# Kernel optimization log

Hardware: AMD Instinct MI355X
Metric: run time of the kernel (lower is better)

The kernel has to match this reference:

```python
import jax, jax.numpy as jnp
import numpy as np

B, T, D, E, K = 4, 1024, 512, 10, 2
H = 4 * D          # expert hidden
CITY, CE = 8, 32   # num cities, city embedding dim
LIN = D + CE + D // 4 + D // 4 + D // 8 + D // 8  # 928 router input dim


def setup_inputs() -> dict:
    key = jax.random.key(0)
    ks = jax.random.split(key, 16)
    s = 0.02  # init scale for weights
    return {
        "x": jax.random.normal(ks[0], (B, T, D), jnp.float32),
        "delta_t": jax.random.normal(ks[1], (B, T, D // 4), jnp.float32),
        "delta_dis": jax.random.normal(ks[2], (B, T, D // 4), jnp.float32),
        "delta_rg": jax.random.normal(ks[3], (B, T, D // 8), jnp.float32),
        "delta_entropy": jax.random.normal(ks[4], (B, T, D // 8), jnp.float32),
        "city_emb": jax.random.normal(ks[5], (CITY, CE), jnp.float32),
        "Wg": jax.random.normal(ks[6], (E, LIN), jnp.float32) * s,
        "bg": jnp.zeros((E,), jnp.float32),
        "Wn": jax.random.normal(ks[7], (E, LIN), jnp.float32) * s,
        "bn": jnp.zeros((E,), jnp.float32),
        "W1": jax.random.normal(ks[8], (E, D, H), jnp.float32) * s,
        "b1": jnp.zeros((E, H), jnp.float32),
        "W2": jax.random.normal(ks[9], (E, H, D), jnp.float32) * s,
        "b2": jnp.zeros((E, D), jnp.float32),
        "noise": jax.random.normal(ks[10], (B, T, E), jnp.float32),
        "city": jax.random.randint(ks[11], (B,), 0, CITY),
    }


def reference(x, delta_t, delta_dis, delta_rg, delta_entropy, city_emb,
              Wg, bg, Wn, bn, W1, b1, W2, b2, noise, city):
    # ---- router: concat features -> noisy top-k gating ----
    ce = city_emb[city]                                   # (B, CE)
    ce = jnp.broadcast_to(ce[:, None, :], (x.shape[0], x.shape[1], ce.shape[-1]))
    h = jnp.concatenate([x, ce, delta_t, delta_dis, delta_rg, delta_entropy], axis=-1)  # (B,T,LIN)
    logits = jnp.einsum('btl,el->bte', h, Wg) + bg        # clean gate logits
    gate1 = jax.nn.softmax(logits, axis=-1)               # dense gate (returned for aux loss)
    noise_logits = jnp.einsum('btl,el->bte', h, Wn) + bn
    noisy = logits + noise * jax.nn.softplus(noise_logits)
    _, idx = jax.lax.top_k(noisy, K)                      # (B,T,K)
    sel = jax.nn.one_hot(idx, E, dtype=noisy.dtype).sum(-2) > 0  # (B,T,E) bool
    gating = jax.nn.softmax(jnp.where(sel, noisy, -jnp.inf), axis=-1)  # zeros off top-k

    # ---- experts: dense compute, combine weighted by sparse gate ----
    flat_x = x.reshape(-1, D)                             # (N, D)
    flat_g = gating.reshape(-1, E)                        # (N, E), zero for non-selected
    hid = jax.nn.gelu(jnp.einsum('nd,edh->neh', flat_x, W1) + b1, approximate=False)
    y = jnp.einsum('neh,ehd->ned', hid, W2) + b2          # (N, E, D)
    out = jnp.einsum('ne,ned->nd', flat_g, y).reshape(x.shape)
    return out, gate1
```

## Files before the change

### kernel.cpp

```cpp
#include <hip/hip_runtime.h>
#include <hip/hip_bf16.h>

#define B_      4
#define T_      1024
#define NTOK    4096
#define D_      512
#define E_      10
#define H_      2048
#define LIN_    928
#define TOPK    2
#define BM      128
#define ROWS_CAP 9472
#define TILES_CAP 74

typedef __bf16 bf16x8 __attribute__((ext_vector_type(8)));
typedef float  f32x4  __attribute__((ext_vector_type(4)));
typedef unsigned short ushort8 __attribute__((ext_vector_type(8)));

#define OFF_W1T   0ull
#define SZ_W1T    (10ull*2048*512*2)
#define OFF_W2T   (OFF_W1T + SZ_W1T)
#define SZ_W2T    SZ_W1T
#define OFF_XG    (OFF_W2T + SZ_W2T)
#define SZ_XG     ((size_t)ROWS_CAP*512*2)
#define OFF_HID   (OFF_XG + SZ_XG)
#define SZ_HID    ((size_t)ROWS_CAP*2048*2)
#define OFF_Y     OFF_W1T
#define OFF_TOKE  (OFF_HID + SZ_HID)
#define OFF_TOKG  (OFF_TOKE + 32768)
#define OFF_TROWS (OFF_TOKG + 32768)
#define OFF_RANK  (OFF_TROWS + 32768)
#define OFF_CNT   (OFF_RANK + 32768)

static __device__ __forceinline__ unsigned short f2b(float f) {
  unsigned int u = __float_as_uint(f);
  unsigned int r = (u + 0x7fffu + ((u >> 16) & 1u)) >> 16;
  return (unsigned short)r;
}

static __device__ __forceinline__ float b2f(unsigned short u) {
  return __uint_as_float(((unsigned int)u) << 16);
}

static __device__ __forceinline__ void gld16(const void* g, void* l) {
  __builtin_amdgcn_global_load_lds(
      (const __attribute__((address_space(1))) unsigned int*)g,
      (__attribute__((address_space(3))) unsigned int*)l, 16, 0, 0);
}

struct WconvLds { float t[64][65]; };

static __device__ __forceinline__ void wconv_body(
    const float* __restrict__ src, unsigned short* __restrict__ dst,
    int R, int C, int e, int bx, int by, int tid, WconvLds* W) {
  int c0 = bx << 6, r0 = by << 6;
  int rr = tid >> 4, cc = (tid & 15) << 2;
  const float* s = src + ((size_t)e * R + r0 + rr) * C + c0 + cc;
#pragma unroll
  for (int p = 0; p < 4; p++) {
    float4 v = *(const float4*)(s + (size_t)p * 16 * C);
    W->t[rr + p * 16][cc + 0] = v.x; W->t[rr + p * 16][cc + 1] = v.y;
    W->t[rr + p * 16][cc + 2] = v.z; W->t[rr + p * 16][cc + 3] = v.w;
  }
  __syncthreads();
  int rb = (tid & 7) * 8;
#pragma unroll
  for (int pass = 0; pass < 2; pass++) {
    int wc2 = pass * 32 + (tid >> 3);
    ushort8 o;
#pragma unroll
    for (int i = 0; i < 8; i++) o[i] = f2b(W->t[rb + i][wc2]);
    *(ushort8*)&dst[((size_t)e * C + c0 + wc2) * R + r0 + rb] = o;
  }
}

__global__ __launch_bounds__(256) void prep_k(
    const float* __restrict__ x, const float* __restrict__ dt,
    const float* __restrict__ dd, const float* __restrict__ dr,
    const float* __restrict__ de, const float* __restrict__ cemb,
    const int* __restrict__ city,
    const float* __restrict__ Wg, const float* __restrict__ Wn,
    const float* __restrict__ bg, const float* __restrict__ bn,
    const float* __restrict__ noise,
    const float* __restrict__ W1, const float* __restrict__ W2,
    unsigned short* __restrict__ w1T, unsigned short* __restrict__ w2T,
    float* __restrict__ gate1, int* __restrict__ tok_e,
    float* __restrict__ tok_g, int* __restrict__ ranks,
    int* __restrict__ counts) {
  __shared__ WconvLds W;
  __shared__ int lcnt[E_], lbase[E_];
  int bx = blockIdx.x;
  int tid = threadIdx.x;
  if (bx >= 256) {
    int idx = bx - 256;
    if (idx < 2560) wconv_body(W1, w1T, 512, 2048, idx / 256, idx & 31, (idx >> 5) & 7, tid, &W);
    else { idx -= 2560; wconv_body(W2, w2T, 2048, 512, idx / 256, idx & 7, (idx >> 3) & 31, tid, &W); }
    return;
  }
  if (tid < E_) lcnt[tid] = 0;
  __syncthreads();
  int lane = tid & 63;
  int gw = bx * 4 + (tid >> 6);
  int n0 = gw * 4;
  int cb = city[n0 >> 10];

  float acc[4][20];
#pragma unroll
  for (int j = 0; j < 4; j++)
#pragma unroll
    for (int o = 0; o < 20; o++) acc[j][o] = 0.f;

  {
    float hce = (lane < 32) ? cemb[cb * 32 + lane] : 0.f;
    int c = 512 + (lane & 31);
#pragma unroll
    for (int o = 0; o < 10; o++) {
      float wg = Wg[o * LIN_ + c];
      float wn = Wn[o * LIN_ + c];
#pragma unroll
      for (int j = 0; j < 4; j++) {
        acc[j][o]      = fmaf(hce, wg, acc[j][o]);
        acc[j][10 + o] = fmaf(hce, wn, acc[j][10 + o]);
      }
    }
  }
#pragma unroll
  for (int s = 0; s < 5; s++) {
    const float* hp; int Wd, cofs;
    if      (s == 0) { hp = x;  Wd = 512; cofs = 0;   }
    else if (s == 1) { hp = dt; Wd = 128; cofs = 544; }
    else if (s == 2) { hp = dd; Wd = 128; cofs = 672; }
    else if (s == 3) { hp = dr; Wd = 64;  cofs = 800; }
    else             { hp = de; Wd = 64;  cofs = 864; }
    for (int base = 0; base < Wd; base += 64) {
      int c = cofs + base + lane;
      float wv[20];
#pragma unroll
      for (int o = 0; o < 10; o++) {
        wv[o]      = Wg[o * LIN_ + c];
        wv[10 + o] = Wn[o * LIN_ + c];
      }
      float hv[4];
#pragma unroll
      for (int j = 0; j < 4; j++) hv[j] = hp[(size_t)(n0 + j) * Wd + base + lane];
#pragma unroll
      for (int j = 0; j < 4; j++)
#pragma unroll
        for (int o = 0; o < 20; o++) acc[j][o] = fmaf(hv[j], wv[o], acc[j][o]);
    }
  }
#pragma unroll
  for (int off = 1; off < 64; off <<= 1) {
#pragma unroll
    for (int j = 0; j < 4; j++)
#pragma unroll
      for (int o = 0; o < 20; o++) acc[j][o] += __shfl_xor(acc[j][o], off);
  }
  float sv[20];
#pragma unroll
  for (int o = 0; o < 20; o++) {
    float v = acc[0][o];
    v = (lane == 1) ? acc[1][o] : v;
    v = (lane == 2) ? acc[2][o] : v;
    v = (lane == 3) ? acc[3][o] : v;
    sv[o] = v;
  }
  int n = n0 + lane;
  int i0 = 0, i1 = 0, rr0 = 0, rr1 = 0;
  float gg0 = 0.f, gg1 = 0.f, gate[E_];
#pragma unroll
  for (int o = 0; o < E_; o++) gate[o] = 0.f;
  if (lane < 4) {
    float logits[E_], noisy[E_];
    float mx = -3.4e38f;
#pragma unroll
    for (int o = 0; o < E_; o++) { logits[o] = sv[o] + bg[o]; mx = fmaxf(mx, logits[o]); }
    float ssum = 0.f;
#pragma unroll
    for (int o = 0; o < E_; o++) { gate[o] = expf(logits[o] - mx); ssum += gate[o]; }
    float inv = 1.f / ssum;
#pragma unroll
    for (int o = 0; o < E_; o++) gate[o] *= inv;
#pragma unroll
    for (int o = 0; o < E_; o++) {
      float tt = sv[10 + o] + bn[o];
      float sp = (tt > 20.f) ? tt : log1pf(expf(tt));
      noisy[o] = logits[o] + noise[(size_t)n * E_ + o] * sp;
    }
    float v0 = noisy[0];
#pragma unroll
    for (int o = 1; o < E_; o++) if (noisy[o] > v0) { v0 = noisy[o]; i0 = o; }
    float v1 = -3.4e38f; i1 = -1;
#pragma unroll
    for (int o = 0; o < E_; o++) if (o != i0 && noisy[o] > v1) { v1 = noisy[o]; i1 = o; }
    float ee = expf(v1 - v0);
    gg0 = 1.f / (1.f + ee); gg1 = ee * gg0;
    rr0 = atomicAdd(&lcnt[i0], 1);
    rr1 = atomicAdd(&lcnt[i1], 1);
  }
  __syncthreads();
  if (tid < E_) lbase[tid] = atomicAdd(&counts[tid], lcnt[tid]);
  __syncthreads();
  if (lane < 4) {
    tok_e[2 * n] = i0;  tok_e[2 * n + 1] = i1;
    tok_g[2 * n] = gg0; tok_g[2 * n + 1] = gg1;
    ranks[2 * n]     = lbase[i0] + rr0;
    ranks[2 * n + 1] = lbase[i1] + rr1;
#pragma unroll
    for (int o = 0; o < E_; o++) gate1[(size_t)n * E_ + o] = gate[o];
  }
}

__global__ __launch_bounds__(256) void scatgath_k(
    const float* __restrict__ x, const int* __restrict__ tok_e,
    const int* __restrict__ ranks, const int* __restrict__ counts,
    int* __restrict__ token_rows, unsigned short* __restrict__ xg) {
  int n = blockIdx.x * 4 + (threadIdx.x >> 6);
  int lane = threadIdx.x & 63;
  int e0 = tok_e[2 * n], e1 = tok_e[2 * n + 1];
  int off0 = 0, off1 = 0, off = 0;
#pragma unroll
  for (int k = 0; k < E_; k++) {
    if (k == e0) off0 = off;
    if (k == e1) off1 = off;
    off += ((counts[k] + BM - 1) / BM) * BM;
  }
  int p0 = off0 + ranks[2 * n];
  int p1 = off1 + ranks[2 * n + 1];
  if (lane == 0) { token_rows[2 * n] = p0; token_rows[2 * n + 1] = p1; }
  float4 a = *(const float4*)&x[(size_t)n * D_ + lane * 8];
  float4 b = *(const float4*)&x[(size_t)n * D_ + lane * 8 + 4];
  ushort8 o;
  o[0] = f2b(a.x); o[1] = f2b(a.y); o[2] = f2b(a.z); o[3] = f2b(a.w);
  o[4] = f2b(b.x); o[5] = f2b(b.y); o[6] = f2b(b.z); o[7] = f2b(b.w);
  *(ushort8*)&xg[(size_t)p0 * D_ + lane * 8] = o;
  *(ushort8*)&xg[(size_t)p1 * D_ + lane * 8] = o;
}

template<int KD, int ND, int GX, int MODE>
__global__ __launch_bounds__(256) void gemm_k(
    const unsigned short* __restrict__ A, const unsigned short* __restrict__ BT,
    const float* __restrict__ bias, unsigned short* __restrict__ outb,
    const int* __restrict__ counts) {
  constexpr int BMT = 128, BNT = 128;
  constexpr int NT = KD / 32;
  constexpr int BUFSZ = (BMT + BNT) * 32;
  int nwg = GX * TILES_CAP;
  int fid = blockIdx.y * GX + blockIdx.x;
  int w = (fid & 7) * (nwg >> 3) + (fid >> 3);
  int bxs = w % GX, bys = w / GX;
  int e = -1, row0 = 0;
  {
    int off = 0, tt = 0;
#pragma unroll
    for (int k = 0; k < E_; k++) {
      int nt = (counts[k] + BM - 1) / BM;
      if (bys >= tt && bys < tt + nt) { e = k; row0 = off + (bys - tt) * BM; }
      tt += nt; off += nt * BM;
    }
  }
  if (e < 0) return;
  int n0 = bxs * BNT;
  int tid = threadIdx.x;
  int lane = tid & 63, wid = tid >> 6;
  int wr = wid >> 1, wc = wid & 1;
  __shared__ __align__(16) unsigned short LDS[3][BUFSZ];
  f32x4 acc[4][4] = {};
  const unsigned short* Ab = A + (size_t)row0 * KD;
  const unsigned short* Bb = BT + ((size_t)e * ND + n0) * KD;
  int lrow = lane >> 2, lcol = (lane & 3) * 8;
  int r = lane & 15, g8 = (lane >> 4) * 8;
  const unsigned short* gp[4];
  int loff[4];
#pragma unroll
  for (int i = 0; i < 4; i++) {
    int rowb = (wid + 4 * i) * 16;
    gp[i] = (rowb < BMT) ? Ab + (size_t)(rowb + lrow) * KD + lcol
                         : Bb + (size_t)(rowb - BMT + lrow) * KD + lcol;
    loff[i] = rowb * 32;
  }
  auto stage = [&](int buf) {
    unsigned short* lb = &LDS[0][0] + buf * BUFSZ;
#pragma unroll
    for (int i = 0; i < 4; i++) { gld16(gp[i], lb + loff[i]); gp[i] += 32; }
  };
  stage(0); stage(1);
  int cur = 0, nb = 2;
  for (int t = 0; t < NT; ++t) {
    if (t + 2 < NT) {
      stage(nb);
      asm volatile("s_waitcnt vmcnt(8)" ::: "memory");
    } else if (t + 2 == NT) {
      asm volatile("s_waitcnt vmcnt(4)" ::: "memory");
    } else {
      asm volatile("s_waitcnt vmcnt(0)" ::: "memory");
    }
    asm volatile("s_barrier" ::: "memory");
    const unsigned short* cb2 = &LDS[0][0] + cur * BUFSZ;
    bf16x8 av[4], bv[4];
#pragma unroll
    for (int mi = 0; mi < 4; mi++)
      av[mi] = *(const bf16x8*)&cb2[(wr * 64 + mi * 16 + r) * 32 + g8];
#pragma unroll
    for (int ni = 0; ni < 4; ni++)
      bv[ni] = *(const bf16x8*)&cb2[(BMT + wc * 64 + ni * 16 + r) * 32 + g8];
#pragma unroll
    for (int mi = 0; mi < 4; mi++)
#pragma unroll
      for (int ni = 0; ni < 4; ni++)
        acc[mi][ni] = __builtin_amdgcn_mfma_f32_16x16x32_bf16(av[mi], bv[ni], acc[mi][ni], 0, 0, 0);
    asm volatile("s_barrier" ::: "memory");
    cur = (cur == 2) ? 0 : cur + 1;
    nb = (nb == 2) ? 0 : nb + 1;
  }
  int rq = (lane >> 4) * 4;
#pragma unroll
  for (int mi = 0; mi < 4; mi++) {
#pragma unroll
    for (int ni = 0; ni < 4; ni++) {
      int col = n0 + wc * 64 + ni * 16 + r;
      float bz = (MODE == 0) ? bias[e * ND + col] : 0.f;
#pragma unroll
      for (int q = 0; q < 4; q++) {
        int row = row0 + wr * 64 + mi * 16 + rq + q;
        float v = acc[mi][ni][q];
        if constexpr (MODE == 0) {
          v += bz;
          v = 0.5f * v * (1.f + erff(v * 0.70710678118654752440f));
        }
        outb[(size_t)row * ND + col] = f2b(v);
      }
    }
  }
}

__global__ void combine_k(const unsigned short* __restrict__ y, const float* __restrict__ b2,
                          const int* __restrict__ token_rows, const int* __restrict__ tok_e,
                          const float* __restrict__ tok_g, float* __restrict__ out) {
  int gid = blockIdx.x * 256 + threadIdx.x;
  int n = gid >> 6;
  int c = (gid & 63) << 3;
  int r0 = token_rows[2 * n], r1 = token_rows[2 * n + 1];
  int e0 = tok_e[2 * n], e1 = tok_e[2 * n + 1];
  float g0 = tok_g[2 * n], g1 = tok_g[2 * n + 1];
  ushort8 y0 = *(const ushort8*)&y[(size_t)r0 * D_ + c];
  ushort8 y1 = *(const ushort8*)&y[(size_t)r1 * D_ + c];
  float ba[8], bb[8], o[8];
  *(float4*)&ba[0] = *(const float4*)&b2[e0 * D_ + c];
  *(float4*)&ba[4] = *(const float4*)&b2[e0 * D_ + c + 4];
  *(float4*)&bb[0] = *(const float4*)&b2[e1 * D_ + c];
  *(float4*)&bb[4] = *(const float4*)&b2[e1 * D_ + c + 4];
#pragma unroll
  for (int j = 0; j < 8; j++)
    o[j] = g0 * (b2f(y0[j]) + ba[j]) + g1 * (b2f(y1[j]) + bb[j]);
  *(float4*)&out[(size_t)n * D_ + c]     = *(float4*)&o[0];
  *(float4*)&out[(size_t)n * D_ + c + 4] = *(float4*)&o[4];
}

extern "C" void kernel_launch(void* const* d_in, const int* in_sizes, int n_in,
                              void* d_out, int out_size, void* d_ws, size_t ws_size,
                              hipStream_t stream) {
  const float* x     = (const float*)d_in[0];
  const float* dt    = (const float*)d_in[1];
  const float* dd    = (const float*)d_in[2];
  const float* dr    = (const float*)d_in[3];
  const float* de    = (const float*)d_in[4];
  const float* cemb  = (const float*)d_in[5];
  const float* Wg    = (const float*)d_in[6];
  const float* bg    = (const float*)d_in[7];
  const float* Wn    = (const float*)d_in[8];
  const float* bn    = (const float*)d_in[9];
  const float* W1    = (const float*)d_in[10];
  const float* b1    = (const float*)d_in[11];
  const float* W2    = (const float*)d_in[12];
  const float* b2    = (const float*)d_in[13];
  const float* noise = (const float*)d_in[14];
  const int*   city  = (const int*)d_in[15];

  float* out   = (float*)d_out;
  float* gate1 = out + (size_t)NTOK * D_;

  char* ws = (char*)d_ws;
  unsigned short* w1T  = (unsigned short*)(ws + OFF_W1T);
  unsigned short* w2T  = (unsigned short*)(ws + OFF_W2T);
  unsigned short* xg   = (unsigned short*)(ws + OFF_XG);
  unsigned short* hid  = (unsigned short*)(ws + OFF_HID);
  unsigned short* yb16 = (unsigned short*)(ws + OFF_Y);
  int*    tok_e       = (int*)(ws + OFF_TOKE);
  float*  tok_g       = (float*)(ws + OFF_TOKG);
  int*    token_rows  = (int*)(ws + OFF_TROWS);
  int*    ranks       = (int*)(ws + OFF_RANK);
  int*    counts      = (int*)(ws + OFF_CNT);

  hipMemsetAsync(counts, 0, E_ * sizeof(int), stream);
  prep_k<<<5376, 256, 0, stream>>>(x, dt, dd, dr, de, cemb, city, Wg, Wn, bg, bn,
                                   noise, W1, W2, w1T, w2T, gate1, tok_e, tok_g,
                                   ranks, counts);
  scatgath_k<<<1024, 256, 0, stream>>>(x, tok_e, ranks, counts, token_rows, xg);
  gemm_k<512, 2048, 16, 0><<<dim3(16, TILES_CAP), 256, 0, stream>>>(xg, w1T, b1, hid, counts);
  gemm_k<2048, 512, 4, 1><<<dim3(4, TILES_CAP), 256, 0, stream>>>(hid, w2T, nullptr, yb16, counts);
  combine_k<<<1024, 256, 0, stream>>>(yb16, b2, token_rows, tok_e, tok_g, out);
}
```

Before: 135.4 us.

## Split router into logit pass and separate top-k kernel, widen weight-convert tiles

The prep kernel now only computes the 20 router logits per token, using 2 tokens per wave instead of 4, and stores them to scratch in the hidden buffer. A new small kernel does the softmax, noisy top-2, gating and per-expert rank assignment with one thread per token, instead of only 4 active lanes per wave. The weight fp32-to-bf16 transpose tiles grow from 64x64 to 64x128, halving the convert block count. This trades an extra kernel launch and a global round trip for the logits against more parallelism in the router dot products and fewer, larger conversion blocks.

```diff
diff --git a/kernel.cpp b/kernel.cpp
--- a/kernel.cpp
+++ b/kernel.cpp
@@ -48,25 +48,26 @@
       (__attribute__((address_space(3))) unsigned int*)l, 16, 0, 0);
 }
 
-struct WconvLds { float t[64][65]; };
+struct WconvLds { float t[64][129]; };
 
 static __device__ __forceinline__ void wconv_body(
     const float* __restrict__ src, unsigned short* __restrict__ dst,
     int R, int C, int e, int bx, int by, int tid, WconvLds* W) {
-  int c0 = bx << 6, r0 = by << 6;
-  int rr = tid >> 4, cc = (tid & 15) << 2;
-  const float* s = src + ((size_t)e * R + r0 + rr) * C + c0 + cc;
-#pragma unroll
-  for (int p = 0; p < 4; p++) {
-    float4 v = *(const float4*)(s + (size_t)p * 16 * C);
-    W->t[rr + p * 16][cc + 0] = v.x; W->t[rr + p * 16][cc + 1] = v.y;
-    W->t[rr + p * 16][cc + 2] = v.z; W->t[rr + p * 16][cc + 3] = v.w;
+  int c0 = bx << 7, r0 = by << 6;
+  int rr = tid >> 5, cc4 = (tid & 31) << 2;
+  const float* s = src + ((size_t)e * R + r0 + rr) * C + c0 + cc4;
+#pragma unroll
+  for (int p = 0; p < 8; p++) {
+    float4 v = *(const float4*)(s + (size_t)p * 8 * C);
+    int row = rr + p * 8;
+    W->t[row][cc4 + 0] = v.x; W->t[row][cc4 + 1] = v.y;
+    W->t[row][cc4 + 2] = v.z; W->t[row][cc4 + 3] = v.w;
   }
   __syncthreads();
   int rb = (tid & 7) * 8;
 #pragma unroll
-  for (int pass = 0; pass < 2; pass++) {
-    int wc2 = pass * 32 + (tid >> 3);
+  for (int p = 0; p < 4; p++) {
+    int wc2 = p * 32 + (tid >> 3);
     ushort8 o;
 #pragma unroll
     for (int i = 0; i < 8; i++) o[i] = f2b(W->t[rb + i][wc2]);
@@ -80,33 +81,32 @@
     const float* __restrict__ de, const float* __restrict__ cemb,
     const int* __restrict__ city,
     const float* __restrict__ Wg, const float* __restrict__ Wn,
-    const float* __restrict__ bg, const float* __restrict__ bn,
-    const float* __restrict__ noise,
     const float* __restrict__ W1, const float* __restrict__ W2,
     unsigned short* __restrict__ w1T, unsigned short* __restrict__ w2T,
-    float* __restrict__ gate1, int* __restrict__ tok_e,
-    float* __restrict__ tok_g, int* __restrict__ ranks,
-    int* __restrict__ counts) {
+    float* __restrict__ logits_all) {
   __shared__ WconvLds W;
-  __shared__ int lcnt[E_], lbase[E_];
   int bx = blockIdx.x;
   int tid = threadIdx.x;
-  if (bx >= 256) {
-    int idx = bx - 256;
-    if (idx < 2560) wconv_body(W1, w1T, 512, 2048, idx / 256, idx & 31, (idx >> 5) & 7, tid, &W);
-    else { idx -= 2560; wconv_body(W2, w2T, 2048, 512, idx / 256, idx & 7, (idx >> 3) & 31, tid, &W); }
+  if (bx >= 512) {
+    int idx = bx - 512;
+    if (idx < 1280) {
+      int e = idx >> 7, rem = idx & 127;
+      wconv_body(W1, w1T, 512, 2048, e, rem & 15, rem >> 4, tid, &W);
+    } else {
+      idx -= 1280;
+      int e = idx >> 7, rem = idx & 127;
+      wconv_body(W2, w2T, 2048, 512, e, rem & 3, rem >> 2, tid, &W);
+    }
     return;
   }
-  if (tid < E_) lcnt[tid] = 0;
-  __syncthreads();
   int lane = tid & 63;
   int gw = bx * 4 + (tid >> 6);
-  int n0 = gw * 4;
+  int n0 = gw * 2;
   int cb = city[n0 >> 10];
 
-  float acc[4][20];
-#pragma unroll
-  for (int j = 0; j < 4; j++)
+  float acc[2][20];
+#pragma unroll
+  for (int j = 0; j < 2; j++)
 #pragma unroll
     for (int o = 0; o < 20; o++) acc[j][o] = 0.f;
 
@@ -118,7 +118,7 @@
       float wg = Wg[o * LIN_ + c];
       float wn = Wn[o * LIN_ + c];
 #pragma unroll
-      for (int j = 0; j < 4; j++) {
+      for (int j = 0; j < 2; j++) {
         acc[j][o]      = fmaf(hce, wg, acc[j][o]);
         acc[j][10 + o] = fmaf(hce, wn, acc[j][10 + o]);
       }
@@ -140,11 +140,11 @@
         wv[o]      = Wg[o * LIN_ + c];
         wv[10 + o] = Wn[o * LIN_ + c];
       }
-      float hv[4];
-#pragma unroll
-      for (int j = 0; j < 4; j++) hv[j] = hp[(size_t)(n0 + j) * Wd + base + lane];
-#pragma unroll
-      for (int j = 0; j < 4; j++)
+      float hv[2];
+#pragma unroll
+      for (int j = 0; j < 2; j++) hv[j] = hp[(size_t)(n0 + j) * Wd + base + lane];
+#pragma unroll
+      for (int j = 0; j < 2; j++)
 #pragma unroll
         for (int o = 0; o < 20; o++) acc[j][o] = fmaf(hv[j], wv[o], acc[j][o]);
     }
@@ -152,63 +152,65 @@
 #pragma unroll
   for (int off = 1; off < 64; off <<= 1) {
 #pragma unroll
-    for (int j = 0; j < 4; j++)
+    for (int j = 0; j < 2; j++)
 #pragma unroll
       for (int o = 0; o < 20; o++) acc[j][o] += __shfl_xor(acc[j][o], off);
   }
-  float sv[20];
-#pragma unroll
-  for (int o = 0; o < 20; o++) {
-    float v = acc[0][o];
-    v = (lane == 1) ? acc[1][o] : v;
-    v = (lane == 2) ? acc[2][o] : v;
-    v = (lane == 3) ? acc[3][o] : v;
-    sv[o] = v;
-  }
-  int n = n0 + lane;
-  int i0 = 0, i1 = 0, rr0 = 0, rr1 = 0;
-  float gg0 = 0.f, gg1 = 0.f, gate[E_];
-#pragma unroll
-  for (int o = 0; o < E_; o++) gate[o] = 0.f;
-  if (lane < 4) {
-    float logits[E_], noisy[E_];
-    float mx = -3.4e38f;
-#pragma unroll
-    for (int o = 0; o < E_; o++) { logits[o] = sv[o] + bg[o]; mx = fmaxf(mx, logits[o]); }
-    float ssum = 0.f;
-#pragma unroll
-    for (int o = 0; o < E_; o++) { gate[o] = expf(logits[o] - mx); ssum += gate[o]; }
-    float inv = 1.f / ssum;
-#pragma unroll
-    for (int o = 0; o < E_; o++) gate[o] *= inv;
-#pragma unroll
-    for (int o = 0; o < E_; o++) {
-      float tt = sv[10 + o] + bn[o];
-      float sp = (tt > 20.f) ? tt : log1pf(expf(tt));
-      noisy[o] = logits[o] + noise[(size_t)n * E_ + o] * sp;
-    }
-    float v0 = noisy[0];
-#pragma unroll
-    for (int o = 1; o < E_; o++) if (noisy[o] > v0) { v0 = noisy[o]; i0 = o; }
-    float v1 = -3.4e38f; i1 = -1;
-#pragma unroll
-    for (int o = 0; o < E_; o++) if (o != i0 && noisy[o] > v1) { v1 = noisy[o]; i1 = o; }
-    float ee = expf(v1 - v0);
-    gg0 = 1.f / (1.f + ee); gg1 = ee * gg0;
-    rr0 = atomicAdd(&lcnt[i0], 1);
-    rr1 = atomicAdd(&lcnt[i1], 1);
-  }
+#pragma unroll
+  for (int j = 0; j < 2; j++) {
+    float v = 0.f;
+#pragma unroll
+    for (int o = 0; o < 20; o++) if (lane == o) v = acc[j][o];
+    if (lane < 20) logits_all[(size_t)(n0 + j) * 20 + lane] = v;
+  }
+}
+
+__global__ __launch_bounds__(256) void route2_k(
+    const float* __restrict__ logits_all,
+    const float* __restrict__ bg, const float* __restrict__ bn,
+    const float* __restrict__ noise,
+    float* __restrict__ gate1, int* __restrict__ tok_e,
+    float* __restrict__ tok_g, int* __restrict__ ranks,
+    int* __restrict__ counts) {
+  __shared__ int lcnt[E_], lbase[E_];
+  int tid = threadIdx.x;
+  if (tid < E_) lcnt[tid] = 0;
+  __syncthreads();
+  int n = blockIdx.x * 256 + tid;
+  const float* p = &logits_all[(size_t)n * 20];
+  float logits[E_], noisy[E_], ex[E_];
+  float mx = -3.4e38f;
+#pragma unroll
+  for (int e = 0; e < E_; e++) { logits[e] = p[e] + bg[e]; mx = fmaxf(mx, logits[e]); }
+  float s = 0.f;
+#pragma unroll
+  for (int e = 0; e < E_; e++) { ex[e] = expf(logits[e] - mx); s += ex[e]; }
+  float invs = 1.f / s;
+#pragma unroll
+  for (int e = 0; e < E_; e++) gate1[(size_t)n * E_ + e] = ex[e] * invs;
+#pragma unroll
+  for (int e = 0; e < E_; e++) {
+    float t = p[10 + e] + bn[e];
+    float sp = (t > 20.f) ? t : log1pf(expf(t));
+    noisy[e] = logits[e] + noise[(size_t)n * E_ + e] * sp;
+  }
+  int i0 = 0; float v0 = noisy[0];
+#pragma unroll
+  for (int e = 1; e < E_; e++) if (noisy[e] > v0) { v0 = noisy[e]; i0 = e; }
+  int i1 = -1; float v1 = -3.4e38f;
+#pragma unroll
+  for (int e = 0; e < E_; e++) if (e != i0 && noisy[e] > v1) { v1 = noisy[e]; i1 = e; }
+  float ee = expf(v1 - v0);
+  float g0 = 1.f / (1.f + ee);
+  tok_e[2 * n] = i0; tok_e[2 * n + 1] = i1;
+  tok_g[2 * n] = g0; tok_g[2 * n + 1] = ee * g0;
+  int r0 = atomicAdd(&lcnt[i0], 1);
+  int r1 = atomicAdd(&lcnt[i1], 1);
   __syncthreads();
   if (tid < E_) lbase[tid] = atomicAdd(&counts[tid], lcnt[tid]);
   __syncthreads();
-  if (lane < 4) {
-    tok_e[2 * n] = i0;  tok_e[2 * n + 1] = i1;
-    tok_g[2 * n] = gg0; tok_g[2 * n + 1] = gg1;
-    ranks[2 * n]     = lbase[i0] + rr0;
-    ranks[2 * n + 1] = lbase[i1] + rr1;
-#pragma unroll
-    for (int o = 0; o < E_; o++) gate1[(size_t)n * E_ + o] = gate[o];
-  }
+  ranks[2 * n]     = lbase[i0] + r0;
+  ranks[2 * n + 1] = lbase[i1] + r1;
 }
 
 __global__ __launch_bounds__(256) void scatgath_k(
@@ -391,10 +393,12 @@
   int*    token_rows  = (int*)(ws + OFF_TROWS);
   int*    ranks       = (int*)(ws + OFF_RANK);
   int*    counts      = (int*)(ws + OFF_CNT);
+  float*  logits_all  = (float*)(ws + OFF_HID);
 
   hipMemsetAsync(counts, 0, E_ * sizeof(int), stream);
-  prep_k<<<5376, 256, 0, stream>>>(x, dt, dd, dr, de, cemb, city, Wg, Wn, bg, bn,
-                                   noise, W1, W2, w1T, w2T, gate1, tok_e, tok_g,
+  prep_k<<<3072, 256, 0, stream>>>(x, dt, dd, dr, de, cemb, city, Wg, Wn,
+                                   W1, W2, w1T, w2T, logits_all);
+  route2_k<<<16, 256, 0, stream>>>(logits_all, bg, bn, noise, gate1, tok_e, tok_g,
                                    ranks, counts);
   scatgath_k<<<1024, 256, 0, stream>>>(x, tok_e, ranks, counts, token_rows, xg);
   gemm_k<512, 2048, 16, 0><<<dim3(16, TILES_CAP), 256, 0, stream>>>(xg, w1T, b1, hid, counts);
```

Result: faster. 122.9 us (-9.3%).
